# Kernel optimization log

Measured on AMD Instinct MI355X. Metric: run time of the kernel, lower is better.

## Reference

```python
import jax, jax.numpy as jnp
import numpy as np

ALPHA = 1.0

def setup_inputs() -> dict:
    key = jax.random.key(0)
    k1, k2 = jax.random.split(key)
    N, D, K = 262144, 64, 256
    x = jax.random.normal(k1, (N, D), dtype=jnp.float32)
    clusters = jax.random.normal(k2, (K, D), dtype=jnp.float32)
    return {"x": x, "clusters": clusters}

def reference(x, clusters):
    # Pairwise squared distances via GEMM decomposition:
    x_sq = jnp.sum(x * x, axis=1, keepdims=True)            # (N, 1)
    c_sq = jnp.sum(clusters * clusters, axis=1)             # (K,)
    cross = x @ clusters.T                                  # (N, K)
    sq_dist = x_sq - 2.0 * cross + c_sq[None, :]            # (N, K)
    # Student-t kernel
    q = 1.0 / (1.0 + sq_dist / ALPHA)
    q = q ** ((ALPHA + 1.0) / 2.0)
    # Row normalize
    q = q / jnp.sum(q, axis=1, keepdims=True)
    return q
```

## Files before the change

### kernel.cpp

```cpp
#include <hip/hip_runtime.h>

#define NKC 256
#define ND  64

using v8bf = __attribute__((ext_vector_type(8))) __bf16;
using v4f  = __attribute__((ext_vector_type(4))) float;
using v4u  = __attribute__((ext_vector_type(4))) unsigned int;

__global__ __launch_bounds__(512, 4)
void cluster_kernel(const float* __restrict__ x,
                    const float* __restrict__ clusters,
                    float* __restrict__ out) {
    __shared__ __align__(16) unsigned short sc[NKC * ND];
    __shared__ float scsq[NKC];
    __shared__ __align__(16) float tsc[8 * 1024];

    const int t    = threadIdx.x;
    const int lane = t & 63;
    const int wid  = t >> 6;
    const int lr   = lane & 15;
    const int hi   = lane >> 4;
    const int kg   = hi << 3;

    const int row = blockIdx.x * 128 + wid * 16 + lr;
    const float* xp = x + (size_t)row * ND + kg;
    v4f x00 = *(const v4f*)(xp);
    v4f x01 = *(const v4f*)(xp + 4);
    v4f x10 = *(const v4f*)(xp + 32);
    v4f x11 = *(const v4f*)(xp + 36);

    {
        const int seg  = t & 3;
        const int rloc = t >> 2;
#pragma unroll
        for (int it = 0; it < 2; ++it) {
            const int crow = it * 128 + rloc;
            const float* cp = clusters + crow * ND + seg * 16;
            v4f c0 = *(const v4f*)(cp);
            v4f c1 = *(const v4f*)(cp + 4);
            v4f c2 = *(const v4f*)(cp + 8);
            v4f c3 = *(const v4f*)(cp + 12);
            float cv[16];
            *(v4f*)&cv[0] = c0; *(v4f*)&cv[4] = c1;
            *(v4f*)&cv[8] = c2; *(v4f*)&cv[12] = c3;
            float ss = 0.f;
#pragma unroll
            for (int i = 0; i < 16; ++i) ss += cv[i] * cv[i];
            ss += __shfl_xor(ss, 1);
            ss += __shfl_xor(ss, 2);
            if (seg == 0) scsq[crow] = ss;
            v8bf w0, w1;
#pragma unroll
            for (int i = 0; i < 8; ++i) {
                w0[i] = (__bf16)cv[i];
                w1[i] = (__bf16)cv[8 + i];
            }
            const int swz = (crow & 7) << 4;
            const int byte0 = crow * 128 + seg * 32;
            *(v8bf*)((char*)sc + ( byte0       ^ swz)) = w0;
            *(v8bf*)((char*)sc + ((byte0 + 16) ^ swz)) = w1;
        }
    }
    __syncthreads();

    float v0[8], v1[8];
    *(v4f*)&v0[0] = x00; *(v4f*)&v0[4] = x01;
    *(v4f*)&v1[0] = x10; *(v4f*)&v1[4] = x11;

    float p = 0.f;
#pragma unroll
    for (int i = 0; i < 8; ++i) p += v0[i] * v0[i] + v1[i] * v1[i];
    p += __shfl_xor(p, 16);
    p += __shfl_xor(p, 32);

    v8bf a0, a1;
#pragma unroll
    for (int i = 0; i < 8; ++i) {
        a0[i] = (__bf16)v0[i];
        a1[i] = (__bf16)v1[i];
    }

    v4f acc[16];
#pragma unroll
    for (int j = 0; j < 16; ++j) {
        const int brow = (j << 4) + lr;
        const int bswz = (brow & 7) << 4;
        v8bf c0 = *(v8bf*)((char*)sc + ((brow * 128      + kg * 2) ^ bswz));
        v8bf c1 = *(v8bf*)((char*)sc + ((brow * 128 + 64 + kg * 2) ^ bswz));
        v4f c = {0.f, 0.f, 0.f, 0.f};
        c = __builtin_amdgcn_mfma_f32_16x16x32_bf16(c0, a0, c, 0, 0, 0);
        c = __builtin_amdgcn_mfma_f32_16x16x32_bf16(c1, a1, c, 0, 0, 0);
        acc[j] = c;
    }

    float ps = 0.f;
#pragma unroll
    for (int j = 0; j < 16; ++j) {
        v4f cs = *(const v4f*)&scsq[(j << 4) + (hi << 2)];
#pragma unroll
        for (int r = 0; r < 4; ++r) {
            float d = p + cs[r] - 2.0f * acc[j][r];
            float u = __builtin_amdgcn_rcpf(1.0f + d);
            acc[j][r] = u;
            ps += u;
        }
    }
    ps += __shfl_xor(ps, 16);
    ps += __shfl_xor(ps, 32);
    const float inv = __builtin_amdgcn_rcpf(ps);
#pragma unroll
    for (int j = 0; j < 16; ++j) {
#pragma unroll
        for (int r = 0; r < 4; ++r) acc[j][r] *= inv;
    }

    char* slice = (char*)tsc + wid * 4096;
    const int q = lr & 3;
    const int rowbase = blockIdx.x * 128 + wid * 16;
#pragma unroll
    for (int rnd = 0; rnd < 4; ++rnd) {
        if ((lr >> 2) == rnd) {
#pragma unroll
            for (int j = 0; j < 16; ++j) {
                *(v4u*)(slice + q * 1024 + (((j ^ q) << 6) + (hi << 4))) =
                    *(v4u*)&acc[j];
            }
        }
        __asm__ volatile("s_waitcnt lgkmcnt(0)" ::: "memory");
#pragma unroll
        for (int q2 = 0; q2 < 4; ++q2) {
            v4u val = *(v4u*)(slice + q2 * 1024 +
                              ((((lane >> 2) ^ q2) << 6) + ((lane & 3) << 4)));
            float* orow = out + (size_t)(rowbase + rnd * 4 + q2) * NKC;
            __builtin_nontemporal_store(val, (v4u*)(orow + (lane << 2)));
        }
        __asm__ volatile("s_waitcnt lgkmcnt(0)" ::: "memory");
    }
}

extern "C" void kernel_launch(void* const* d_in, const int* in_sizes, int n_in,
                              void* d_out, int out_size, void* d_ws, size_t ws_size,
                              hipStream_t stream) {
    const float* x        = (const float*)d_in[0];
    const float* clusters = (const float*)d_in[1];
    float* out = (float*)d_out;
    const int N = in_sizes[0] / ND;

    cluster_kernel<<<N / 128, 512, 0, stream>>>(x, clusters, out);
}
```

Before: 58.21 us.

## Make kernel persistent with grid-stride tiles and prefetch next x tile

Replaces the one-block-per-tile launch with a fixed grid of 512 persistent blocks that loop over 128-row tiles. The bf16 cluster matrix is converted into LDS only once per block instead of once per tile. Each iteration prefetches the next tile's x rows into registers while the current tile runs its epilogue. The intended savings are the repeated cluster staging and the global-load latency, at the cost of higher register pressure and possible load imbalance (2048 tiles over 512 blocks is exactly 4 each).

Result: slower. 88.84 us (+52.6%).

```diff
diff --git a/kernel.cpp b/kernel.cpp
--- a/kernel.cpp
+++ b/kernel.cpp
@@ -10,7 +10,8 @@
 __global__ __launch_bounds__(512, 4)
 void cluster_kernel(const float* __restrict__ x,
                     const float* __restrict__ clusters,
-                    float* __restrict__ out) {
+                    float* __restrict__ out,
+                    int ntiles) {
     __shared__ __align__(16) unsigned short sc[NKC * ND];
     __shared__ float scsq[NKC];
     __shared__ __align__(16) float tsc[8 * 1024];
@@ -21,13 +22,14 @@
     const int lr   = lane & 15;
     const int hi   = lane >> 4;
     const int kg   = hi << 3;
+    const int nblk = gridDim.x;
 
-    const int row = blockIdx.x * 128 + wid * 16 + lr;
-    const float* xp = x + (size_t)row * ND + kg;
-    v4f x00 = *(const v4f*)(xp);
-    v4f x01 = *(const v4f*)(xp + 4);
-    v4f x10 = *(const v4f*)(xp + 32);
-    v4f x11 = *(const v4f*)(xp + 36);
+    int tile = blockIdx.x;
+    const float* xp0 = x + ((size_t)(tile * 128 + wid * 16 + lr)) * ND + kg;
+    v4f nx00 = *(const v4f*)(xp0);
+    v4f nx01 = *(const v4f*)(xp0 + 4);
+    v4f nx10 = *(const v4f*)(xp0 + 32);
+    v4f nx11 = *(const v4f*)(xp0 + 36);
 
     {
         const int seg  = t & 3;
@@ -63,78 +65,94 @@
     }
     __syncthreads();
 
-    float v0[8], v1[8];
-    *(v4f*)&v0[0] = x00; *(v4f*)&v0[4] = x01;
-    *(v4f*)&v1[0] = x10; *(v4f*)&v1[4] = x11;
-
-    float p = 0.f;
-#pragma unroll
-    for (int i = 0; i < 8; ++i) p += v0[i] * v0[i] + v1[i] * v1[i];
-    p += __shfl_xor(p, 16);
-    p += __shfl_xor(p, 32);
-
-    v8bf a0, a1;
-#pragma unroll
-    for (int i = 0; i < 8; ++i) {
-        a0[i] = (__bf16)v0[i];
-        a1[i] = (__bf16)v1[i];
-    }
-
-    v4f acc[16];
-#pragma unroll
-    for (int j = 0; j < 16; ++j) {
-        const int brow = (j << 4) + lr;
-        const int bswz = (brow & 7) << 4;
-        v8bf c0 = *(v8bf*)((char*)sc + ((brow * 128      + kg * 2) ^ bswz));
-        v8bf c1 = *(v8bf*)((char*)sc + ((brow * 128 + 64 + kg * 2) ^ bswz));
-        v4f c = {0.f, 0.f, 0.f, 0.f};
-        c = __builtin_amdgcn_mfma_f32_16x16x32_bf16(c0, a0, c, 0, 0, 0);
-        c = __builtin_amdgcn_mfma_f32_16x16x32_bf16(c1, a1, c, 0, 0, 0);
-        acc[j] = c;
-    }
-
-    float ps = 0.f;
-#pragma unroll
-    for (int j = 0; j < 16; ++j) {
-        v4f cs = *(const v4f*)&scsq[(j << 4) + (hi << 2)];
-#pragma unroll
-        for (int r = 0; r < 4; ++r) {
-            float d = p + cs[r] - 2.0f * acc[j][r];
-            float u = __builtin_amdgcn_rcpf(1.0f + d);
-            acc[j][r] = u;
-            ps += u;
-        }
-    }
-    ps += __shfl_xor(ps, 16);
-    ps += __shfl_xor(ps, 32);
-    const float inv = __builtin_amdgcn_rcpf(ps);
-#pragma unroll
-    for (int j = 0; j < 16; ++j) {
-#pragma unroll
-        for (int r = 0; r < 4; ++r) acc[j][r] *= inv;
-    }
-
     char* slice = (char*)tsc + wid * 4096;
     const int q = lr & 3;
-    const int rowbase = blockIdx.x * 128 + wid * 16;
+
+    while (tile < ntiles) {
+        v4f x00 = nx00, x01 = nx01, x10 = nx10, x11 = nx11;
+        const int next = tile + nblk;
+
+        float v0[8], v1[8];
+        *(v4f*)&v0[0] = x00; *(v4f*)&v0[4] = x01;
+        *(v4f*)&v1[0] = x10; *(v4f*)&v1[4] = x11;
+
+        float p = 0.f;
 #pragma unroll
-    for (int rnd = 0; rnd < 4; ++rnd) {
-        if ((lr >> 2) == rnd) {
+        for (int i = 0; i < 8; ++i) p += v0[i] * v0[i] + v1[i] * v1[i];
+        p += __shfl_xor(p, 16);
+        p += __shfl_xor(p, 32);
+
+        v8bf a0, a1;
 #pragma unroll
-            for (int j = 0; j < 16; ++j) {
-                *(v4u*)(slice + q * 1024 + (((j ^ q) << 6) + (hi << 4))) =
-                    *(v4u*)&acc[j];
+        for (int i = 0; i < 8; ++i) {
+            a0[i] = (__bf16)v0[i];
+            a1[i] = (__bf16)v1[i];
+        }
+
+        v4f acc[16];
+#pragma unroll
+        for (int j = 0; j < 16; ++j) {
+            const int brow = (j << 4) + lr;
+            const int bswz = (brow & 7) << 4;
+            v8bf c0 = *(v8bf*)((char*)sc + ((brow * 128      + kg * 2) ^ bswz));
+            v8bf c1 = *(v8bf*)((char*)sc + ((brow * 128 + 64 + kg * 2) ^ bswz));
+            v4f c = {0.f, 0.f, 0.f, 0.f};
+            c = __builtin_amdgcn_mfma_f32_16x16x32_bf16(c0, a0, c, 0, 0, 0);
+            c = __builtin_amdgcn_mfma_f32_16x16x32_bf16(c1, a1, c, 0, 0, 0);
+            acc[j] = c;
+        }
+
+        if (next < ntiles) {
+            const float* xq = x + ((size_t)(next * 128 + wid * 16 + lr)) * ND + kg;
+            nx00 = *(const v4f*)(xq);
+            nx01 = *(const v4f*)(xq + 4);
+            nx10 = *(const v4f*)(xq + 32);
+            nx11 = *(const v4f*)(xq + 36);
+        }
+
+        float ps = 0.f;
+#pragma unroll
+        for (int j = 0; j < 16; ++j) {
+            v4f cs = *(const v4f*)&scsq[(j << 4) + (hi << 2)];
+#pragma unroll
+            for (int r = 0; r < 4; ++r) {
+                float d = p + cs[r] - 2.0f * acc[j][r];
+                float u = __builtin_amdgcn_rcpf(1.0f + d);
+                acc[j][r] = u;
+                ps += u;
             }
         }
-        __asm__ volatile("s_waitcnt lgkmcnt(0)" ::: "memory");
+        ps += __shfl_xor(ps, 16);
+        ps += __shfl_xor(ps, 32);
+        const float inv = __builtin_amdgcn_rcpf(ps);
 #pragma unroll
-        for (int q2 = 0; q2 < 4; ++q2) {
-            v4u val = *(v4u*)(slice + q2 * 1024 +
-                              ((((lane >> 2) ^ q2) << 6) + ((lane & 3) << 4)));
-            float* orow = out + (size_t)(rowbase + rnd * 4 + q2) * NKC;
-            __builtin_nontemporal_store(val, (v4u*)(orow + (lane << 2)));
+        for (int j = 0; j < 16; ++j) {
+#pragma unroll
+            for (int r = 0; r < 4; ++r) acc[j][r] *= inv;
         }
-        __asm__ volatile("s_waitcnt lgkmcnt(0)" ::: "memory");
+
+        const int rowbase = tile * 128 + wid * 16;
+#pragma unroll
+        for (int rnd = 0; rnd < 4; ++rnd) {
+            if ((lr >> 2) == rnd) {
+#pragma unroll
+                for (int j = 0; j < 16; ++j) {
+                    *(v4u*)(slice + q * 1024 + (((j ^ q) << 6) + (hi << 4))) =
+                        *(v4u*)&acc[j];
+                }
+            }
+            __asm__ volatile("s_waitcnt lgkmcnt(0)" ::: "memory");
+#pragma unroll
+            for (int q2 = 0; q2 < 4; ++q2) {
+                v4u val = *(v4u*)(slice + q2 * 1024 +
+                                  ((((lane >> 2) ^ q2) << 6) + ((lane & 3) << 4)));
+                float* orow = out + (size_t)(rowbase + rnd * 4 + q2) * NKC;
+                __builtin_nontemporal_store(val, (v4u*)(orow + (lane << 2)));
+            }
+            __asm__ volatile("s_waitcnt lgkmcnt(0)" ::: "memory");
+        }
+
+        tile = next;
     }
 }
 
@@ -145,6 +163,7 @@
     const float* clusters = (const float*)d_in[1];
     float* out = (float*)d_out;
     const int N = in_sizes[0] / ND;
+    const int ntiles = N / 128;
 
-    cluster_kernel<<<N / 128, 512, 0, stream>>>(x, clusters, out);
+    cluster_kernel<<<512, 512, 0, stream>>>(x, clusters, out, ntiles);
 }
```
